# Kernel tuning notes

Measured on AMD Instinct MI355X. Metric: run time of the kernel, lower is better.

Reference implementation:

```python
import jax, jax.numpy as jnp
import numpy as np

INF = 1e8
CLIP = 10.0  # clip_logits
H = 128      # hidden/embedding units
D = 3        # embed_dim


def _lstm_cell(x, h, c, Wih, Whh, b):
    # torch LSTM gate order: i, f, g, o
    g = x @ Wih.T + h @ Whh.T + b
    i, f, gg, o = jnp.split(g, 4, axis=-1)
    c = jax.nn.sigmoid(f) * c + jax.nn.sigmoid(i) * jnp.tanh(gg)
    h = jax.nn.sigmoid(o) * jnp.tanh(c)
    return h, c


def setup_inputs() -> dict:
    key = jax.random.key(0)
    ks = jax.random.split(key, 20)
    B, N = 2048, 128
    u = lambda k, shape: jax.random.uniform(k, shape, jnp.float32, -0.08, 0.08)
    return {
        "x": jax.random.normal(ks[0], (B, N, D), jnp.float32),
        "W_embed": u(ks[1], (H, D)),
        "enc_Wih": u(ks[2], (4 * H, H)), "enc_Whh": u(ks[3], (4 * H, H)), "enc_b": u(ks[4], (4 * H,)),
        "dec_Wih": u(ks[5], (4 * H, H)), "dec_Whh": u(ks[6], (4 * H, H)), "dec_b": u(ks[7], (4 * H,)),
        "Wq": u(ks[8], (H, H)), "bq": u(ks[9], (H,)),
        "Wq2": u(ks[10], (H, H)), "bq2": u(ks[11], (H,)),
        "Wref": u(ks[12], (H, H)), "bref": u(ks[13], (H,)),
        "Wref2": u(ks[14], (H, H)), "bref2": u(ks[15], (H,)),
        "Vec": u(ks[16], (H,)), "Vec2": u(ks[17], (H,)),
        "dec_input0": u(ks[18], (H,)),
    }


def reference(x, W_embed, enc_Wih, enc_Whh, enc_b, dec_Wih, dec_Whh, dec_b,
              Wq, bq, Wq2, bq2, Wref, bref, Wref2, bref2, Vec, Vec2, dec_input0):
    B, N, _ = x.shape
    embed = x @ W_embed.T  # (B, N, H)

    # --- Encoder LSTM over the N view points ---
    h0 = jnp.zeros((B, H), x.dtype)
    def enc_step(carry, xt):
        h, c = carry
        h, c = _lstm_cell(xt, h, c, enc_Wih, enc_Whh, enc_b)
        return (h, c), h
    (h, c), hs = jax.lax.scan(enc_step, (h0, h0), jnp.swapaxes(embed, 0, 1))
    ref = jnp.swapaxes(hs, 0, 1)  # (B, N, H) == encoder_h

    # W_ref / W_ref2 are 1x1 convs over a fixed reference -> precompute once
    u2g = ref @ Wref.T + bref    # (B, N, H)
    u2p = ref @ Wref2.T + bref2  # (B, N, H)

    keys = jax.random.split(jax.random.key(42), N)
    mask0 = jnp.zeros((B, N), x.dtype)
    dec_in0 = jnp.broadcast_to(dec_input0, (B, H))

    def dec_step(carry, key):
        h, c, mask, dec_in = carry
        h, c = _lstm_cell(dec_in, h, c, dec_Wih, dec_Whh, dec_b)
        # --- glimpse (num_glimpse = 1) ---
        u1 = h @ Wq.T + bq  # (B, H)
        sc = jnp.einsum('bnh,h->bn', jnp.tanh(u1[:, None, :] + u2g), Vec) - INF * mask
        a = jax.nn.softmax(sc, axis=1)
        q = jnp.einsum('bnh,bn->bh', u2g, a)
        # --- pointer ---
        u1p = q @ Wq2.T + bq2
        logits = jnp.einsum('bnh,h->bn', CLIP * jnp.tanh(u1p[:, None, :] + u2p), Vec2) - INF * mask
        log_p = jax.nn.log_softmax(logits, axis=-1)  # softmax_T = 1
        nxt = jax.random.categorical(key, log_p, axis=-1)  # multinomial sample
        dec_in = jnp.take_along_axis(embed, nxt[:, None, None], axis=1)[:, 0, :]
        mask = mask + jax.nn.one_hot(nxt, N, dtype=mask.dtype)
        return (h, c, mask, dec_in), (nxt, log_p)

    _, (PI_t, logp_t) = jax.lax.scan(dec_step, (h, c, mask0, dec_in0), keys)
    PI = jnp.swapaxes(PI_t, 0, 1)        # (B, N)
    log_ps = jnp.swapaxes(logp_t, 0, 1)  # (B, N, N)
    ll = jnp.take_along_axis(log_ps, PI[:, :, None], axis=2)[..., 0].sum(axis=1)
    return PI, ll
```

## Files before the change

### kernel.cpp

```cpp
#include <hip/hip_runtime.h>
#include <cstdint>
#include <cstddef>


__device__ __forceinline__ float keepf(float v){ asm volatile("" : "+v"(v)); return v; }

__device__ __forceinline__ float xtanh(float x){
  float ax = fabsf(x);
  float xc = fminf(fmaxf(x, -7.90531110763549805f), 7.90531110763549805f);
  float x2 = xc * xc;
  float np = -2.76076847742355e-16f;
  np = fmaf(np, x2, 2.00018790482477e-13f);
  np = fmaf(np, x2, -8.60467152213735e-11f);
  np = fmaf(np, x2, 5.12229709037114e-08f);
  np = fmaf(np, x2, 1.48572235717979e-05f);
  np = fmaf(np, x2, 6.37261928875436e-04f);
  np = fmaf(np, x2, 4.89352455891786e-03f);
  float num = xc * np;
  float dp = 1.19825839466702e-06f;
  dp = fmaf(dp, x2, 1.18534705686654e-04f);
  dp = fmaf(dp, x2, 2.26843463243900e-03f);
  dp = fmaf(dp, x2, 4.89352518554385e-03f);
  float r = num / dp;
  return (ax < 0.0004f) ? x : r;
}

__device__ __forceinline__ float xsig(float x){ return 1.0f / (1.0f + expf(-x)); }

__device__ __forceinline__ void tf2x32(uint32_t k0, uint32_t k1, uint32_t x0, uint32_t x1,
                                       uint32_t& o0, uint32_t& o1){
  const uint32_t ks2 = k0 ^ k1 ^ 0x1BD11BDAu;
  x0 += k0; x1 += k1;
#define RR(r) { x0 += x1; x1 = (x1<<(r))|(x1>>(32-(r))); x1 ^= x0; }
  RR(13) RR(15) RR(26) RR(6)  x0 += k1;  x1 += ks2 + 1u;
  RR(17) RR(29) RR(16) RR(24) x0 += ks2; x1 += k0 + 2u;
  RR(13) RR(15) RR(26) RR(6)  x0 += k0;  x1 += k1 + 3u;
  RR(17) RR(29) RR(16) RR(24) x0 += k1;  x1 += ks2 + 4u;
  RR(13) RR(15) RR(26) RR(6)  x0 += ks2; x1 += k0 + 5u;
#undef RR
  o0 = x0; o1 = x1;
}

__device__ __forceinline__ float gumbel_from(uint32_t k0, uint32_t k1, uint32_t ctr){
  uint32_t a, b; tf2x32(k0, k1, 0u, ctr, a, b);
  uint32_t bits = a ^ b;
  float f = __uint_as_float((bits >> 9) | 0x3F800000u) - 1.0f;
  if (f == 0.0f) f = 1.17549435e-38f;
  return -logf(-logf(f));
}

__global__ void setup_kernel(const float* __restrict__ We, const float* __restrict__ eWih,
                             const float* __restrict__ dWih, const float* __restrict__ dec0,
                             float* __restrict__ M3e, float* __restrict__ M3d, float* __restrict__ g0d){
  int id = blockIdx.x * 256 + threadIdx.x;
  if (id < 1536){
    int oo = id / 3, d = id % 3;
    double a = 0.0;
    for (int k = 0; k < 128; ++k) a += (double)eWih[oo*128+k] * (double)We[k*3+d];
    M3e[oo*4+d] = (float)a;
    if (d == 0) M3e[oo*4+3] = 0.f;
  } else if (id < 3072){
    int id2 = id - 1536; int oo = id2 / 3, d = id2 % 3;
    double a = 0.0;
    for (int k = 0; k < 128; ++k) a += (double)dWih[oo*128+k] * (double)We[k*3+d];
    M3d[oo*4+d] = (float)a;
    if (d == 0) M3d[oo*4+3] = 0.f;
  } else if (id < 3584){
    int oo = id - 3072;
    double a = 0.0;
    for (int k = 0; k < 128; ++k) a += (double)dWih[oo*128+k] * (double)dec0[k];
    g0d[oo] = (float)a;
  }
}

__global__ __launch_bounds__(512, 1) void enc_kernel(
    const float* __restrict__ x, const float* __restrict__ Whh,
    const float* __restrict__ eb, const float* __restrict__ M3,
    float* __restrict__ ref, float* __restrict__ hcfin){
  __shared__ float pred[4][8][512];
  __shared__ float hT[128][8];
  __shared__ float cT[8][128];
  __shared__ float m3s[512][4];
  __shared__ float bs[512];
  __shared__ float xs[8][4];
  const int tid = threadIdx.x;
  const int lane = tid & 63;
  const int b0 = blockIdx.x << 3;

  { int i = tid; bs[i] = eb[i];
    float4 mv = *(const float4*)&M3[i*4]; *(float4*)&m3s[i][0] = mv; }
  for (int i = tid; i < 1024; i += 512){ ((float*)hT)[i] = 0.f; ((float*)cT)[i] = 0.f; }

  const int og = tid & 127, kp = tid >> 7;
  float w[4][32];
#pragma unroll
  for (int c = 0; c < 4; ++c)
#pragma unroll
    for (int i = 0; i < 32; i += 4){
      float4 v = *(const float4*)&Whh[(og*4+c)*128 + kp*32 + i];
      w[c][i] = v.x; w[c][i+1] = v.y; w[c][i+2] = v.z; w[c][i+3] = v.w;
    }
  __syncthreads();

#pragma unroll 1
  for (int t = 0; t < 128; ++t){
    if (tid < 32){ int r = tid >> 2, d = tid & 3;
      xs[r][d] = (d < 3) ? x[((b0+r)*128 + t)*3 + d] : 0.f; }
    float h8[8];
    { int krow = kp*32 + (lane & 31);
      float4 p0 = *(const float4*)&hT[krow][0];
      float4 p1 = *(const float4*)&hT[krow][4];
      h8[0]=p0.x; h8[1]=p0.y; h8[2]=p0.z; h8[3]=p0.w;
      h8[4]=p1.x; h8[5]=p1.y; h8[6]=p1.z; h8[7]=p1.w; }
    float acc[8][4];
#pragma unroll
    for (int r = 0; r < 8; ++r){ acc[r][0]=0.f; acc[r][1]=0.f; acc[r][2]=0.f; acc[r][3]=0.f; }
#pragma unroll
    for (int i = 0; i < 32; ++i){
#pragma unroll
      for (int r = 0; r < 8; ++r){
        float hv = __int_as_float(__builtin_amdgcn_readlane(__float_as_int(h8[r]), i));
        acc[r][0] = fmaf(hv, w[0][i], acc[r][0]);
        acc[r][1] = fmaf(hv, w[1][i], acc[r][1]);
        acc[r][2] = fmaf(hv, w[2][i], acc[r][2]);
        acc[r][3] = fmaf(hv, w[3][i], acc[r][3]);
      }
    }
#pragma unroll
    for (int r = 0; r < 8; ++r){
      float4 v = {acc[r][0], acc[r][1], acc[r][2], acc[r][3]};
      *(float4*)&pred[kp][r][og*4] = v;
    }
    __syncthreads();
    { const int u = tid & 127; const int r0v = (tid >> 7) * 2;
#pragma unroll
      for (int rr = r0v; rr < r0v + 2; ++rr){
        float g[4];
#pragma unroll
        for (int gi = 0; gi < 4; ++gi){
          int oo = u + (gi << 7);
          float hw = ((pred[0][rr][oo] + pred[1][rr][oo]) + pred[2][rr][oo]) + pred[3][rr][oo];
          float xw = fmaf(m3s[oo][2], xs[rr][2], fmaf(m3s[oo][1], xs[rr][1], m3s[oo][0]*xs[rr][0]));
          g[gi] = (xw + hw) + bs[oo];
        }
        float i_ = xsig(g[0]), f_ = xsig(g[1]), gg = xtanh(g[2]), o_ = xsig(g[3]);
        float a1 = keepf(f_ * cT[rr][u]);
        float a2 = keepf(i_ * gg);
        float cn = a1 + a2;
        float hn = o_ * xtanh(cn);
        cT[rr][u] = cn; hT[u][rr] = hn;
        ref[(((size_t)(b0+rr))*128 + t)*128 + u] = hn;
        if (t == 127){ hcfin[(b0+rr)*256 + u] = hn; hcfin[(b0+rr)*256 + 128 + u] = cn; }
      }
    }
    __syncthreads();
  }
}

#define DCHUNK(G, OFF) \
  { float4 uv = *(const float4*)&ub[OFF]; float4 vv = *(const float4*)&vb[OFF]; \
    s = fmaf(xtanh(uv.x + G.x), vv.x, s); \
    s = fmaf(xtanh(uv.y + G.y), vv.y, s); \
    s = fmaf(xtanh(uv.z + G.z), vv.z, s); \
    s = fmaf(xtanh(uv.w + G.w), vv.w, s); }

#define ICHUNK(P, OFF) \
  { float4 uv = *(const float4*)&ub[OFF]; float4 vv = *(const float4*)&vb[OFF]; \
    s = fmaf(10.0f*xtanh(uv.x + P.x), vv.x, s); \
    s = fmaf(10.0f*xtanh(uv.y + P.y), vv.y, s); \
    s = fmaf(10.0f*xtanh(uv.z + P.z), vv.z, s); \
    s = fmaf(10.0f*xtanh(uv.w + P.w), vv.w, s); }

__global__ __launch_bounds__(512)
__attribute__((amdgpu_waves_per_eu(2)))
void dec_kernel(
    const float* __restrict__ x,
    const float* __restrict__ Whh, const float* __restrict__ db,
    const float* __restrict__ Wq, const float* __restrict__ bq,
    const float* __restrict__ Wq2, const float* __restrict__ bq2,
    const float* __restrict__ Wref, const float* __restrict__ bref,
    const float* __restrict__ Wref2, const float* __restrict__ bref2,
    const float* __restrict__ Vec, const float* __restrict__ Vec2,
    const float* __restrict__ M3, const float* __restrict__ g0,
    const float* __restrict__ ref, const float* __restrict__ hcfin,
    float* __restrict__ out){
  __shared__ __align__(16) float u2g[128][132];
  __shared__ __align__(16) float scratch[16896];
  __shared__ float gbuf[512];
  __shared__ float hbuf[128], cbuf[128], scb[128], lpb[128], maskf[128], abuf[128];
  __shared__ float bqb[128], bq2b[128];
  __shared__ uint32_t keyx[128], keyy[128];
  __shared__ float xrb[4];
  const int tid = threadIdx.x;
  const int lane = tid & 63;
  const int wv = tid >> 6;
  const int b = blockIdx.x;

  if (tid < 128){
    uint32_t a, bb; tf2x32(0u, 42u, 0u, (uint32_t)tid, a, bb);
    keyx[tid] = a; keyy[tid] = bb;
    hbuf[tid] = hcfin[b*256 + tid];
    cbuf[tid] = hcfin[b*256 + 128 + tid];
    maskf[tid] = 0.f;
    bqb[tid] = bq[tid];   bq2b[tid] = bq2[tid];
  }
  {
    const int j = tid & 127, m = (tid >> 7) & 1, th = tid >> 8;
    const float* W = m ? Wref2 : Wref;
    const float bj = m ? bref2[j] : bref[j];
    float wrow[128];
#pragma unroll
    for (int k = 0; k < 128; k += 4){ float4 v = *(const float4*)&W[j*128+k];
      wrow[k]=v.x; wrow[k+1]=v.y; wrow[k+2]=v.z; wrow[k+3]=v.w; }
    float* dst = m ? scratch : &u2g[0][0];
#pragma unroll 1
    for (int t = th*64; t < th*64 + 64; ++t){
      const float* rr = ref + (((size_t)b)*128 + t)*128;
      float a = 0.f;
#pragma unroll
      for (int k = 0; k < 128; ++k) a = fmaf(wrow[k], rr[k], a);
      dst[t*132 + j] = a + bj;
    }
  }
  __syncthreads();

  const int n_ = tid >> 2, hp = tid & 3;
  const float* gsrc = &u2g[n_][hp*32];
  const float* psrc = &scratch[n_*132 + hp*32];
  float4 G0 = *(const float4*)&gsrc[0],  G1 = *(const float4*)&gsrc[4];
  float4 G2 = *(const float4*)&gsrc[8],  G3 = *(const float4*)&gsrc[12];
  float4 G4 = *(const float4*)&gsrc[16], G5 = *(const float4*)&gsrc[20];
  float4 G6 = *(const float4*)&gsrc[24], G7 = *(const float4*)&gsrc[28];
  float4 P0 = *(const float4*)&psrc[0],  P1 = *(const float4*)&psrc[4];
  float4 P2 = *(const float4*)&psrc[8],  P3 = *(const float4*)&psrc[12];
  float4 P4 = *(const float4*)&psrc[16], P5 = *(const float4*)&psrc[20];
  float4 P6 = *(const float4*)&psrc[24], P7 = *(const float4*)&psrc[28];
  __syncthreads();

  float* hrep   = scratch;
  float* u1rep  = scratch + 544;
  float* qrep   = scratch + 1088;
  float* u1prep = scratch + 1632;
  float* vrep   = scratch + 2176;
  float* v2rep  = scratch + 2720;
  float* qpart  = scratch + 3264;

  if (tid < 128){
    float v1 = Vec[tid], v2 = Vec2[tid];
#pragma unroll
    for (int r = 0; r < 4; ++r){ vrep[r*136+tid] = v1; v2rep[r*136+tid] = v2; }
  }

  const int o = tid;
  const float* __restrict__ wr = Whh + o*128;
  const float bo = db[o];
  float4 m4 = *(const float4*)&M3[o*4];
  const float g0o = g0[o];
  float llacc = 0.f;
  __syncthreads();

#pragma unroll 1
  for (int t = 0; t < 128; ++t){
    {
      float h0v = hbuf[lane], h1v = hbuf[64+lane];
      float acc = 0.f;
#pragma unroll
      for (int k = 0; k < 64; k += 4){
        float4 w4 = *(const float4*)&wr[k];
        float hv;
        hv = __int_as_float(__builtin_amdgcn_readlane(__float_as_int(h0v), k));   acc = fmaf(hv, w4.x, acc);
        hv = __int_as_float(__builtin_amdgcn_readlane(__float_as_int(h0v), k+1)); acc = fmaf(hv, w4.y, acc);
        hv = __int_as_float(__builtin_amdgcn_readlane(__float_as_int(h0v), k+2)); acc = fmaf(hv, w4.z, acc);
        hv = __int_as_float(__builtin_amdgcn_readlane(__float_as_int(h0v), k+3)); acc = fmaf(hv, w4.w, acc);
      }
#pragma unroll
      for (int k = 0; k < 64; k += 4){
        float4 w4 = *(const float4*)&wr[64 + k];
        float hv;
        hv = __int_as_float(__builtin_amdgcn_readlane(__float_as_int(h1v), k));   acc = fmaf(hv, w4.x, acc);
        hv = __int_as_float(__builtin_amdgcn_readlane(__float_as_int(h1v), k+1)); acc = fmaf(hv, w4.y, acc);
        hv = __int_as_float(__builtin_amdgcn_readlane(__float_as_int(h1v), k+2)); acc = fmaf(hv, w4.z, acc);
        hv = __int_as_float(__builtin_amdgcn_readlane(__float_as_int(h1v), k+3)); acc = fmaf(hv, w4.w, acc);
      }
      float xw = (t == 0) ? g0o : fmaf(m4.z, xrb[2], fmaf(m4.y, xrb[1], m4.x*xrb[0]));
      gbuf[o] = (xw + acc) + bo;
    }
    __syncthreads();
    if (tid < 128){
      float gi = gbuf[tid], gf = gbuf[128+tid], gg = gbuf[256+tid], go = gbuf[384+tid];
      float i_ = xsig(gi), f_ = xsig(gf), g_ = xtanh(gg), o_ = xsig(go);
      float a1 = keepf(f_ * cbuf[tid]);
      float a2 = keepf(i_ * g_);
      float cn = a1 + a2;
      float hn = o_ * xtanh(cn);
      cbuf[tid] = cn; hbuf[tid] = hn;
#pragma unroll
      for (int r = 0; r < 4; ++r) hrep[r*136 + tid] = hn;
    }
    __syncthreads();
    {
      const int j = tid >> 2, kp = tid & 3;
      const float* hb = hrep + kp*136;
      float a = 0.f;
#pragma unroll
      for (int i = 0; i < 32; i += 4){
        float4 wv4 = *(const float4*)&Wq[j*128 + kp*32 + i];
        float4 hv4 = *(const float4*)&hb[kp*32 + i];
        a = fmaf(wv4.x,hv4.x,a); a = fmaf(wv4.y,hv4.y,a); a = fmaf(wv4.z,hv4.z,a); a = fmaf(wv4.w,hv4.w,a);
      }
      a += __shfl_xor(a, 1);
      a += __shfl_xor(a, 2);
      u1rep[kp*136 + j] = a + bqb[j];
    }
    __syncthreads();
    {
      const float* ub = u1rep + hp*136 + hp*32;
      const float* vb = vrep  + hp*136 + hp*32;
      float s = 0.f;
      DCHUNK(G0, 0)  DCHUNK(G1, 4)  DCHUNK(G2, 8)  DCHUNK(G3, 12)
      DCHUNK(G4, 16) DCHUNK(G5, 20) DCHUNK(G6, 24) DCHUNK(G7, 28)
      s += __shfl_xor(s, 1);
      s += __shfl_xor(s, 2);
      if (hp == 0){ float mm = keepf(1e8f * maskf[n_]); scb[n_] = s - mm; }
    }
    __syncthreads();
    {
      float v0 = scb[lane], v1 = scb[64+lane];
      float mx = fmaxf(v0, v1);
#pragma unroll
      for (int d2 = 1; d2 < 64; d2 <<= 1) mx = fmaxf(mx, __shfl_xor(mx, d2));
      float e0 = expf(v0 - mx), e1 = expf(v1 - mx);
      float sm = e0 + e1;
#pragma unroll
      for (int d2 = 1; d2 < 64; d2 <<= 1) sm += __shfl_xor(sm, d2);
      abuf[lane] = e0 / sm;
      abuf[64+lane] = e1 / sm;
    }
    {
      const int hc = tid & 31, np = tid >> 5;
      float q0=0.f,q1=0.f,q2=0.f,q3=0.f;
#pragma unroll
      for (int jj = 0; jj < 8; ++jj){
        int n = np*8 + jj;
        float an = abuf[n];
        float4 ug = *(const float4*)&u2g[n][hc*4];
        q0 = fmaf(an, ug.x, q0); q1 = fmaf(an, ug.y, q1);
        q2 = fmaf(an, ug.z, q2); q3 = fmaf(an, ug.w, q3);
      }
      float4 qv = {q0,q1,q2,q3};
      *(float4*)&qpart[np*128 + hc*4] = qv;
    }
    __syncthreads();
    if (tid < 128){
      float s = qpart[tid];
#pragma unroll
      for (int np = 1; np < 16; ++np) s += qpart[np*128 + tid];
#pragma unroll
      for (int r = 0; r < 4; ++r) qrep[r*136 + tid] = s;
    }
    __syncthreads();
    {
      const int j = tid >> 2, kp = tid & 3;
      const float* qb = qrep + kp*136;
      float a = 0.f;
#pragma unroll
      for (int i = 0; i < 32; i += 4){
        float4 wv4 = *(const float4*)&Wq2[j*128 + kp*32 + i];
        float4 hv4 = *(const float4*)&qb[kp*32 + i];
        a = fmaf(wv4.x,hv4.x,a); a = fmaf(wv4.y,hv4.y,a); a = fmaf(wv4.z,hv4.z,a); a = fmaf(wv4.w,hv4.w,a);
      }
      a += __shfl_xor(a, 1);
      a += __shfl_xor(a, 2);
      u1prep[kp*136 + j] = a + bq2b[j];
    }
    __syncthreads();
    {
      const float* ub = u1prep + hp*136 + hp*32;
      const float* vb = v2rep  + hp*136 + hp*32;
      float s = 0.f;
      ICHUNK(P0, 0)  ICHUNK(P1, 4)  ICHUNK(P2, 8)  ICHUNK(P3, 12)
      ICHUNK(P4, 16) ICHUNK(P5, 20) ICHUNK(P6, 24) ICHUNK(P7, 28)
      s += __shfl_xor(s, 1);
      s += __shfl_xor(s, 2);
      if (hp == 0){ float mm = keepf(1e8f * maskf[n_]); scb[n_] = s - mm; }
    }
    __syncthreads();
    if (wv == 0){
      float v0 = scb[lane], v1 = scb[64+lane];
      float mx = fmaxf(v0, v1);
#pragma unroll
      for (int d2 = 1; d2 < 64; d2 <<= 1) mx = fmaxf(mx, __shfl_xor(mx, d2));
      float s0 = v0 - mx, s1 = v1 - mx;
      float e0 = expf(s0), e1 = expf(s1);
      float sm = e0 + e1;
#pragma unroll
      for (int d2 = 1; d2 < 64; d2 <<= 1) sm += __shfl_xor(sm, d2);
      float lz = logf(sm);
      float lp0 = s0 - lz, lp1 = s1 - lz;
      lpb[lane] = lp0; lpb[64+lane] = lp1;
      float gv0 = gumbel_from(keyx[t], keyy[t], (uint32_t)(b*128 + lane));
      float gv1 = gumbel_from(keyx[t], keyy[t], (uint32_t)(b*128 + 64 + lane));
      float val0 = gv0 + lp0, val1 = gv1 + lp1;
      float bv; int bi;
      if (val1 > val0){ bv = val1; bi = 64 + lane; } else { bv = val0; bi = lane; }
#pragma unroll
      for (int d2 = 1; d2 < 64; d2 <<= 1){
        float ov = __shfl_xor(bv, d2);
        int   oi = __shfl_xor(bi, d2);
        if (ov > bv || (ov == bv && oi < bi)){ bv = ov; bi = oi; }
      }
      if (lane == 0){
        out[b*128 + t] = (float)bi;
        llacc += lpb[bi];
        maskf[bi] = 1.f;
      }
      if (lane < 3) xrb[lane] = x[((size_t)(b*128 + bi))*3 + lane];
    }
    __syncthreads();
  }
  if (tid == 0) out[262144 + b] = llacc;
}

extern "C" void kernel_launch(void* const* d_in, const int* in_sizes, int n_in,
                              void* d_out, int out_size, void* d_ws, size_t ws_size,
                              hipStream_t stream){
  (void)in_sizes; (void)n_in; (void)out_size; (void)ws_size;
  const float* x        = (const float*)d_in[0];
  const float* W_embed  = (const float*)d_in[1];
  const float* enc_Wih  = (const float*)d_in[2];
  const float* enc_Whh  = (const float*)d_in[3];
  const float* enc_b    = (const float*)d_in[4];
  const float* dec_Wih  = (const float*)d_in[5];
  const float* dec_Whh  = (const float*)d_in[6];
  const float* dec_b    = (const float*)d_in[7];
  const float* Wq       = (const float*)d_in[8];
  const float* bq       = (const float*)d_in[9];
  const float* Wq2      = (const float*)d_in[10];
  const float* bq2      = (const float*)d_in[11];
  const float* Wref     = (const float*)d_in[12];
  const float* bref     = (const float*)d_in[13];
  const float* Wref2    = (const float*)d_in[14];
  const float* bref2    = (const float*)d_in[15];
  const float* Vec      = (const float*)d_in[16];
  const float* Vec2     = (const float*)d_in[17];
  const float* dec0     = (const float*)d_in[18];
  float* out = (float*)d_out;
  char* ws = (char*)d_ws;
  float* ref   = (float*)(ws);
  float* hcfin = (float*)(ws + 134217728);
  float* M3e   = (float*)(ws + 136314880);
  float* M3d   = (float*)(ws + 136323072);
  float* g0d   = (float*)(ws + 136331264);

  setup_kernel<<<14, 256, 0, stream>>>(W_embed, enc_Wih, dec_Wih, dec0, M3e, M3d, g0d);
  enc_kernel<<<256, 512, 0, stream>>>(x, enc_Whh, enc_b, M3e, ref, hcfin);
  dec_kernel<<<2048, 512, 0, stream>>>(x, dec_Whh, dec_b, Wq, bq, Wq2, bq2,
                                       Wref, bref, Wref2, bref2, Vec, Vec2,
                                       M3d, g0d, ref, hcfin, out);
}
```

Baseline: 18.52 ms.

## Shrink decoder LDS footprint and drop register-cached glimpse projections for occupancy

Removes the waves_per_eu hint and cuts shared memory by reusing one small region for gate, h, query and score buffers. The glimpse projection u2g is no longer cached in registers but read from LDS each step, and the key schedule and log-prob buffer are recomputed or shuffled instead of stored. Wref/Wref2 projections are recomputed with an 8-row register tiled loop rather than a 128-float weight row per thread. Together these aim to lower LDS and VGPR pressure so more blocks fit per CU. The cost is extra LDS reads, cross-slot reductions with additional barriers, and per-step Threefry key recomputation.

```diff
diff --git a/kernel.cpp b/kernel.cpp
--- a/kernel.cpp
+++ b/kernel.cpp
@@ -157,13 +157,6 @@
   }
 }
 
-#define DCHUNK(G, OFF) \
-  { float4 uv = *(const float4*)&ub[OFF]; float4 vv = *(const float4*)&vb[OFF]; \
-    s = fmaf(xtanh(uv.x + G.x), vv.x, s); \
-    s = fmaf(xtanh(uv.y + G.y), vv.y, s); \
-    s = fmaf(xtanh(uv.z + G.z), vv.z, s); \
-    s = fmaf(xtanh(uv.w + G.w), vv.w, s); }
-
 #define ICHUNK(P, OFF) \
   { float4 uv = *(const float4*)&ub[OFF]; float4 vv = *(const float4*)&vb[OFF]; \
     s = fmaf(10.0f*xtanh(uv.x + P.x), vv.x, s); \
@@ -171,8 +164,12 @@
     s = fmaf(10.0f*xtanh(uv.z + P.z), vv.z, s); \
     s = fmaf(10.0f*xtanh(uv.w + P.w), vv.w, s); }
 
+#define PRO4(ACC, ROW) \
+  { float4 r4 = *(const float4*)&(ROW)[kc*4]; \
+    ACC = fmaf(w4.x, r4.x, ACC); ACC = fmaf(w4.y, r4.y, ACC); \
+    ACC = fmaf(w4.z, r4.z, ACC); ACC = fmaf(w4.w, r4.w, ACC); }
+
 __global__ __launch_bounds__(512)
-__attribute__((amdgpu_waves_per_eu(2)))
 void dec_kernel(
     const float* __restrict__ x,
     const float* __restrict__ Whh, const float* __restrict__ db,
@@ -184,71 +181,78 @@
     const float* __restrict__ M3, const float* __restrict__ g0,
     const float* __restrict__ ref, const float* __restrict__ hcfin,
     float* __restrict__ out){
-  __shared__ __align__(16) float u2g[128][132];
-  __shared__ __align__(16) float scratch[16896];
-  __shared__ float gbuf[512];
-  __shared__ float hbuf[128], cbuf[128], scb[128], lpb[128], maskf[128], abuf[128];
+  __shared__ __align__(16) float u2g[16896];
+  __shared__ __align__(16) float region[2176];
+  __shared__ float vecb[128], vec2b[128];
+  __shared__ float hbuf[128], cbuf[128], scb[128], maskf[128], abuf[128];
   __shared__ float bqb[128], bq2b[128];
-  __shared__ uint32_t keyx[128], keyy[128];
   __shared__ float xrb[4];
   const int tid = threadIdx.x;
   const int lane = tid & 63;
   const int wv = tid >> 6;
   const int b = blockIdx.x;
+  const int SLOT1 = 544, SLOT2 = 1088, SLOT3 = 1632;
 
   if (tid < 128){
-    uint32_t a, bb; tf2x32(0u, 42u, 0u, (uint32_t)tid, a, bb);
-    keyx[tid] = a; keyy[tid] = bb;
     hbuf[tid] = hcfin[b*256 + tid];
     cbuf[tid] = hcfin[b*256 + 128 + tid];
     maskf[tid] = 0.f;
     bqb[tid] = bq[tid];   bq2b[tid] = bq2[tid];
-  }
+    vecb[tid] = Vec[tid]; vec2b[tid] = Vec2[tid];
+  }
+
   {
-    const int j = tid & 127, m = (tid >> 7) & 1, th = tid >> 8;
-    const float* W = m ? Wref2 : Wref;
-    const float bj = m ? bref2[j] : bref[j];
-    float wrow[128];
-#pragma unroll
-    for (int k = 0; k < 128; k += 4){ float4 v = *(const float4*)&W[j*128+k];
-      wrow[k]=v.x; wrow[k+1]=v.y; wrow[k+2]=v.z; wrow[k+3]=v.w; }
-    float* dst = m ? scratch : &u2g[0][0];
+    const int j = tid & 127, th = tid >> 7;
+    const float bj = bref2[j];
+    const float* Wr = Wref2 + j*128;
 #pragma unroll 1
-    for (int t = th*64; t < th*64 + 64; ++t){
-      const float* rr = ref + (((size_t)b)*128 + t)*128;
-      float a = 0.f;
-#pragma unroll
-      for (int k = 0; k < 128; ++k) a = fmaf(wrow[k], rr[k], a);
-      dst[t*132 + j] = a + bj;
+    for (int g = 0; g < 4; ++g){
+      const int t0 = th*32 + g*8;
+      const float* rb = ref + (((size_t)b)*128 + t0)*128;
+      float a0=0.f,a1=0.f,a2=0.f,a3=0.f,a4=0.f,a5=0.f,a6=0.f,a7=0.f;
+#pragma unroll
+      for (int kc = 0; kc < 32; ++kc){
+        float4 w4 = *(const float4*)&Wr[kc*4];
+        PRO4(a0, rb + 0*128) PRO4(a1, rb + 1*128) PRO4(a2, rb + 2*128) PRO4(a3, rb + 3*128)
+        PRO4(a4, rb + 4*128) PRO4(a5, rb + 5*128) PRO4(a6, rb + 6*128) PRO4(a7, rb + 7*128)
+      }
+      u2g[(t0+0)*132 + j] = a0 + bj; u2g[(t0+1)*132 + j] = a1 + bj;
+      u2g[(t0+2)*132 + j] = a2 + bj; u2g[(t0+3)*132 + j] = a3 + bj;
+      u2g[(t0+4)*132 + j] = a4 + bj; u2g[(t0+5)*132 + j] = a5 + bj;
+      u2g[(t0+6)*132 + j] = a6 + bj; u2g[(t0+7)*132 + j] = a7 + bj;
     }
   }
   __syncthreads();
-
-  const int n_ = tid >> 2, hp = tid & 3;
-  const float* gsrc = &u2g[n_][hp*32];
-  const float* psrc = &scratch[n_*132 + hp*32];
-  float4 G0 = *(const float4*)&gsrc[0],  G1 = *(const float4*)&gsrc[4];
-  float4 G2 = *(const float4*)&gsrc[8],  G3 = *(const float4*)&gsrc[12];
-  float4 G4 = *(const float4*)&gsrc[16], G5 = *(const float4*)&gsrc[20];
-  float4 G6 = *(const float4*)&gsrc[24], G7 = *(const float4*)&gsrc[28];
-  float4 P0 = *(const float4*)&psrc[0],  P1 = *(const float4*)&psrc[4];
-  float4 P2 = *(const float4*)&psrc[8],  P3 = *(const float4*)&psrc[12];
-  float4 P4 = *(const float4*)&psrc[16], P5 = *(const float4*)&psrc[20];
-  float4 P6 = *(const float4*)&psrc[24], P7 = *(const float4*)&psrc[28];
+  const int hp2 = tid >> 7, n2 = tid & 127;
+  float4 P0, P1, P2, P3, P4, P5, P6, P7;
+  {
+    const float* ps = u2g + n2*132 + hp2*32;
+    P0 = *(const float4*)&ps[0];  P1 = *(const float4*)&ps[4];
+    P2 = *(const float4*)&ps[8];  P3 = *(const float4*)&ps[12];
+    P4 = *(const float4*)&ps[16]; P5 = *(const float4*)&ps[20];
+    P6 = *(const float4*)&ps[24]; P7 = *(const float4*)&ps[28];
+  }
   __syncthreads();
-
-  float* hrep   = scratch;
-  float* u1rep  = scratch + 544;
-  float* qrep   = scratch + 1088;
-  float* u1prep = scratch + 1632;
-  float* vrep   = scratch + 2176;
-  float* v2rep  = scratch + 2720;
-  float* qpart  = scratch + 3264;
-
-  if (tid < 128){
-    float v1 = Vec[tid], v2 = Vec2[tid];
-#pragma unroll
-    for (int r = 0; r < 4; ++r){ vrep[r*136+tid] = v1; v2rep[r*136+tid] = v2; }
+  {
+    const int j = tid & 127, th = tid >> 7;
+    const float bj = bref[j];
+    const float* Wr = Wref + j*128;
+#pragma unroll 1
+    for (int g = 0; g < 4; ++g){
+      const int t0 = th*32 + g*8;
+      const float* rb = ref + (((size_t)b)*128 + t0)*128;
+      float a0=0.f,a1=0.f,a2=0.f,a3=0.f,a4=0.f,a5=0.f,a6=0.f,a7=0.f;
+#pragma unroll
+      for (int kc = 0; kc < 32; ++kc){
+        float4 w4 = *(const float4*)&Wr[kc*4];
+        PRO4(a0, rb + 0*128) PRO4(a1, rb + 1*128) PRO4(a2, rb + 2*128) PRO4(a3, rb + 3*128)
+        PRO4(a4, rb + 4*128) PRO4(a5, rb + 5*128) PRO4(a6, rb + 6*128) PRO4(a7, rb + 7*128)
+      }
+      u2g[(t0+0)*132 + j] = a0 + bj; u2g[(t0+1)*132 + j] = a1 + bj;
+      u2g[(t0+2)*132 + j] = a2 + bj; u2g[(t0+3)*132 + j] = a3 + bj;
+      u2g[(t0+4)*132 + j] = a4 + bj; u2g[(t0+5)*132 + j] = a5 + bj;
+      u2g[(t0+6)*132 + j] = a6 + bj; u2g[(t0+7)*132 + j] = a7 + bj;
+    }
   }
 
   const int o = tid;
@@ -283,11 +287,11 @@
         hv = __int_as_float(__builtin_amdgcn_readlane(__float_as_int(h1v), k+3)); acc = fmaf(hv, w4.w, acc);
       }
       float xw = (t == 0) ? g0o : fmaf(m4.z, xrb[2], fmaf(m4.y, xrb[1], m4.x*xrb[0]));
-      gbuf[o] = (xw + acc) + bo;
+      region[o] = (xw + acc) + bo;
     }
     __syncthreads();
     if (tid < 128){
-      float gi = gbuf[tid], gf = gbuf[128+tid], gg = gbuf[256+tid], go = gbuf[384+tid];
+      float gi = region[tid], gf = region[128+tid], gg = region[256+tid], go = region[384+tid];
       float i_ = xsig(gi), f_ = xsig(gf), g_ = xtanh(gg), o_ = xsig(go);
       float a1 = keepf(f_ * cbuf[tid]);
       float a2 = keepf(i_ * g_);
@@ -295,12 +299,12 @@
       float hn = o_ * xtanh(cn);
       cbuf[tid] = cn; hbuf[tid] = hn;
 #pragma unroll
-      for (int r = 0; r < 4; ++r) hrep[r*136 + tid] = hn;
+      for (int r = 0; r < 4; ++r) region[SLOT1 + r*136 + tid] = hn;
     }
     __syncthreads();
     {
       const int j = tid >> 2, kp = tid & 3;
-      const float* hb = hrep + kp*136;
+      const float* hb = region + SLOT1 + kp*136;
       float a = 0.f;
 #pragma unroll
       for (int i = 0; i < 32; i += 4){
@@ -310,18 +314,33 @@
       }
       a += __shfl_xor(a, 1);
       a += __shfl_xor(a, 2);
-      u1rep[kp*136 + j] = a + bqb[j];
-    }
-    __syncthreads();
-    {
-      const float* ub = u1rep + hp*136 + hp*32;
-      const float* vb = vrep  + hp*136 + hp*32;
+      if (kp == 0) region[SLOT2 + j] = a + bqb[j];
+    }
+    __syncthreads();
+    {
+      const float* ub = region + SLOT2 + hp2*32;
+      const float* vb = vecb + hp2*32;
+      const float* gp = u2g + n2*132 + hp2*32;
       float s = 0.f;
-      DCHUNK(G0, 0)  DCHUNK(G1, 4)  DCHUNK(G2, 8)  DCHUNK(G3, 12)
-      DCHUNK(G4, 16) DCHUNK(G5, 20) DCHUNK(G6, 24) DCHUNK(G7, 28)
-      s += __shfl_xor(s, 1);
-      s += __shfl_xor(s, 2);
-      if (hp == 0){ float mm = keepf(1e8f * maskf[n_]); scb[n_] = s - mm; }
+#pragma unroll
+      for (int i = 0; i < 32; i += 4){
+        float4 uv = *(const float4*)&ub[i];
+        float4 vv = *(const float4*)&vb[i];
+        float4 g4 = *(const float4*)&gp[i];
+        s = fmaf(xtanh(uv.x + g4.x), vv.x, s);
+        s = fmaf(xtanh(uv.y + g4.y), vv.y, s);
+        s = fmaf(xtanh(uv.z + g4.z), vv.z, s);
+        s = fmaf(xtanh(uv.w + g4.w), vv.w, s);
+      }
+      region[SLOT3 + hp2*132 + n2] = s;
+    }
+    __syncthreads();
+    if (tid < 128){
+      float t1 = region[SLOT3 + tid] + region[SLOT3 + 132 + tid];
+      float t2 = region[SLOT3 + 264 + tid] + region[SLOT3 + 396 + tid];
+      float ss = t1 + t2;
+      float mm = keepf(1e8f * maskf[tid]);
+      scb[tid] = ss - mm;
     }
     __syncthreads();
     {
@@ -343,25 +362,29 @@
       for (int jj = 0; jj < 8; ++jj){
         int n = np*8 + jj;
         float an = abuf[n];
-        float4 ug = *(const float4*)&u2g[n][hc*4];
+        float4 ug = *(const float4*)&u2g[n*132 + hc*4];
         q0 = fmaf(an, ug.x, q0); q1 = fmaf(an, ug.y, q1);
         q2 = fmaf(an, ug.z, q2); q3 = fmaf(an, ug.w, q3);
       }
       float4 qv = {q0,q1,q2,q3};
-      *(float4*)&qpart[np*128 + hc*4] = qv;
-    }
-    __syncthreads();
+      *(float4*)&region[np*128 + hc*4] = qv;
+    }
+    __syncthreads();
+    float qs = 0.f;
     if (tid < 128){
-      float s = qpart[tid];
-#pragma unroll
-      for (int np = 1; np < 16; ++np) s += qpart[np*128 + tid];
-#pragma unroll
-      for (int r = 0; r < 4; ++r) qrep[r*136 + tid] = s;
+      qs = region[tid];
+#pragma unroll
+      for (int np = 1; np < 16; ++np) qs += region[np*128 + tid];
+    }
+    __syncthreads();
+    if (tid < 128){
+#pragma unroll
+      for (int r = 0; r < 4; ++r) region[r*136 + tid] = qs;
     }
     __syncthreads();
     {
       const int j = tid >> 2, kp = tid & 3;
-      const float* qb = qrep + kp*136;
+      const float* qb = region + kp*136;
       float a = 0.f;
 #pragma unroll
       for (int i = 0; i < 32; i += 4){
@@ -371,18 +394,24 @@
       }
       a += __shfl_xor(a, 1);
       a += __shfl_xor(a, 2);
-      u1prep[kp*136 + j] = a + bq2b[j];
-    }
-    __syncthreads();
-    {
-      const float* ub = u1prep + hp*136 + hp*32;
-      const float* vb = v2rep  + hp*136 + hp*32;
+      if (kp == 0) region[SLOT1 + j] = a + bq2b[j];
+    }
+    __syncthreads();
+    {
+      const float* ub = region + SLOT1 + hp2*32;
+      const float* vb = vec2b + hp2*32;
       float s = 0.f;
       ICHUNK(P0, 0)  ICHUNK(P1, 4)  ICHUNK(P2, 8)  ICHUNK(P3, 12)
       ICHUNK(P4, 16) ICHUNK(P5, 20) ICHUNK(P6, 24) ICHUNK(P7, 28)
-      s += __shfl_xor(s, 1);
-      s += __shfl_xor(s, 2);
-      if (hp == 0){ float mm = keepf(1e8f * maskf[n_]); scb[n_] = s - mm; }
+      region[SLOT3 + hp2*132 + n2] = s;
+    }
+    __syncthreads();
+    if (tid < 128){
+      float t1 = region[SLOT3 + tid] + region[SLOT3 + 132 + tid];
+      float t2 = region[SLOT3 + 264 + tid] + region[SLOT3 + 396 + tid];
+      float ss = t1 + t2;
+      float mm = keepf(1e8f * maskf[tid]);
+      scb[tid] = ss - mm;
     }
     __syncthreads();
     if (wv == 0){
@@ -397,9 +426,9 @@
       for (int d2 = 1; d2 < 64; d2 <<= 1) sm += __shfl_xor(sm, d2);
       float lz = logf(sm);
       float lp0 = s0 - lz, lp1 = s1 - lz;
-      lpb[lane] = lp0; lpb[64+lane] = lp1;
-      float gv0 = gumbel_from(keyx[t], keyy[t], (uint32_t)(b*128 + lane));
-      float gv1 = gumbel_from(keyx[t], keyy[t], (uint32_t)(b*128 + 64 + lane));
+      uint32_t kx, ky; tf2x32(0u, 42u, 0u, (uint32_t)t, kx, ky);
+      float gv0 = gumbel_from(kx, ky, (uint32_t)(b*128 + lane));
+      float gv1 = gumbel_from(kx, ky, (uint32_t)(b*128 + 64 + lane));
       float val0 = gv0 + lp0, val1 = gv1 + lp1;
       float bv; int bi;
       if (val1 > val0){ bv = val1; bi = 64 + lane; } else { bv = val0; bi = lane; }
@@ -409,9 +438,12 @@
         int   oi = __shfl_xor(bi, d2);
         if (ov > bv || (ov == bv && oi < bi)){ bv = ov; bi = oi; }
       }
+      float lpa = __shfl(lp0, bi & 63);
+      float lpbv = __shfl(lp1, bi & 63);
+      float lpsel = (bi < 64) ? lpa : lpbv;
       if (lane == 0){
         out[b*128 + t] = (float)bi;
-        llacc += lpb[bi];
+        llacc += lpsel;
         maskf[bi] = 1.f;
       }
       if (lane < 3) xrb[lane] = x[((size_t)(b*128 + bi))*3 + lane];
```

Result: faster. 17.22 ms (-7.0%).
